# Kernel tuning notes

Measured on AMD Instinct MI355X. Metric: run time of the kernel, lower is better.

The kernel has to match this reference:

```python
import jax, jax.numpy as jnp
import numpy as np

N = 100_000      # nodes
E = 3_200_000    # edges (avg degree 32)
HID = 64         # hid_dim == in_dim
T = 4            # S2V propagation rounds


def setup_inputs() -> dict:
    key = jax.random.key(0)
    ks = jax.random.split(key, 10)
    s = lambda fan: 1.0 / np.sqrt(fan)
    return {
        "x": jax.random.normal(ks[0], (N, HID), jnp.float32),
        "x_tag": jax.random.uniform(ks[1], (N,), jnp.float32),
        "edge_attr": jax.random.uniform(ks[2], (E, 1), jnp.float32),
        "edge_index": jax.random.randint(ks[3], (2, E), 0, N, dtype=jnp.int32),
        # per-layer bias-free Linear weights (stored as [in, out])
        "W1": jax.random.normal(ks[4], (T, HID), jnp.float32),            # lin1: 1 -> hid
        "W2": jax.random.normal(ks[5], (T, HID, HID), jnp.float32) * s(HID),  # lin2: in -> hid
        "W4": jax.random.normal(ks[6], (T, HID), jnp.float32),            # lin4: 1 -> hid
        "W5": jax.random.normal(ks[7], (2 * HID, 1), jnp.float32) * s(2 * HID),  # lin5
        "W6": jax.random.normal(ks[8], (HID, HID), jnp.float32) * s(HID),  # lin6
        "W7": jax.random.normal(ks[9], (HID, HID), jnp.float32) * s(HID),  # lin7
    }


def reference(x, x_tag, edge_attr, edge_index, W1, W2, W4, W5, W6, W7):
    src = edge_index[0]  # j (message source / p3 scatter target)
    dst = edge_index[1]  # i (aggregation target)
    for l in range(T):  # fixed small layer count
        p1 = x_tag[:, None] * W1[l][None, :]                        # lin1(x_tag)  [N,HID]
        e = jax.nn.relu(edge_attr * W4[l][None, :])                  # relu(lin4(edge_attr)) [E,HID]
        aggr = jax.ops.segment_sum(x[src], dst, num_segments=N)     # add-aggregate x_j at i
        p2 = aggr @ W2[l]                                            # lin2(aggr_out)
        p3 = jax.ops.segment_sum(e, src, num_segments=N)             # scatter_add at edge_index[0]
        x = jax.nn.relu(p1 + p2 + p3)
    graph_pool = jnp.sum(x, axis=0, keepdims=True) @ W6              # [1,HID]
    nodes_vec = x @ W7                                               # [N,HID]
    cat = jnp.concatenate(
        [jnp.broadcast_to(graph_pool, (x.shape[0], graph_pool.shape[1])), nodes_vec], axis=1
    )
    Q = jax.nn.relu(cat) @ W5                                        # [N,1]
    return Q
```

## Files before the change

### kernel.cpp

```cpp
#include <hip/hip_runtime.h>

constexpr int NN  = 100000;
constexpr int NE  = 3200000;
constexpr int HID = 64;
constexpr int TL  = 4;

constexpr int BIN_SHIFT = 9;
constexpr int BIN_NODES = 1 << BIN_SHIFT;
constexpr int NBINS     = (NN + BIN_NODES - 1) / BIN_NODES;
constexpr int BINCAP    = 18944;
constexpr int TILE_E    = 2048;
constexpr int PAD       = 48;
constexpr int LROW      = 72;

typedef unsigned short ushort_t;
typedef unsigned int uint_t;
typedef __attribute__((ext_vector_type(8))) short bf16x8;
typedef __attribute__((ext_vector_type(4))) float f32x4;

__device__ __forceinline__ ushort_t f2b(float f) {
  uint_t u = __float_as_uint(f);
  u += 0x7fff + ((u >> 16) & 1);
  return (ushort_t)(u >> 16);
}
__device__ __forceinline__ float b2f(ushort_t h) {
  return __uint_as_float(((uint_t)h) << 16);
}

__global__ __launch_bounds__(256) void escatter_kernel(
    const int* __restrict__ ei, const float* __restrict__ ea,
    int* __restrict__ bincursor, uint_t* __restrict__ gbin,
    int* __restrict__ bincursor2, uint_t* __restrict__ gbin2) {
  __shared__ int hist1[256], hist2[256];
  __shared__ int base1[NBINS], base2[NBINS];
  __shared__ int offs1[NBINS], offs2[NBINS];
  __shared__ int wt1[4], wt2[4];
  __shared__ uint_t srec[TILE_E];
  __shared__ int    sdst[TILE_E];
  int tid = threadIdx.x;
  int tb = blockIdx.x * TILE_E;
  hist1[tid] = 0; hist2[tid] = 0;
  __syncthreads();
  uint_t rec1[8], rec2[8]; int bn1[8], bn2[8], rk1[8], rk2[8];
  #pragma unroll
  for (int j = 0; j < 8; ++j) {
    int e = tb + tid + j * 256;
    bn1[j] = -1; bn2[j] = -1;
    rk1[j] = 0; rk2[j] = 0; rec1[j] = 0; rec2[j] = 0;
    if (e < NE) {
      int s = ei[e];
      int d = ei[NE + e];
      uint_t q = (uint_t)(int)(ea[e] * 8388608.0f);
      bn1[j] = d >> BIN_SHIFT;
      rec1[j] = ((uint_t)s << BIN_SHIFT) | (uint_t)(d & (BIN_NODES - 1));
      rk1[j] = atomicAdd(&hist1[bn1[j]], 1);
      bn2[j] = s >> BIN_SHIFT;
      rec2[j] = (q << BIN_SHIFT) | (uint_t)(s & (BIN_NODES - 1));
      rk2[j] = atomicAdd(&hist2[bn2[j]], 1);
    }
  }
  __syncthreads();
  int c1 = hist1[tid], c2 = hist2[tid];
  int lane = tid & 63;
  int wvx = tid >> 6;
  int v1 = c1, v2 = c2;
  #pragma unroll
  for (int o = 1; o < 64; o <<= 1) {
    int t1 = __shfl_up(v1, o);
    int t2 = __shfl_up(v2, o);
    if (lane >= o) { v1 += t1; v2 += t2; }
  }
  if (lane == 63) { wt1[wvx] = v1; wt2[wvx] = v2; }
  __syncthreads();
  for (int k = 0; k < wvx; ++k) { v1 += wt1[k]; v2 += wt2[k]; }
  hist1[tid] = v1; hist2[tid] = v2;
  __syncthreads();
  if (tid < NBINS) {
    offs1[tid] = hist1[tid] - c1;
    offs2[tid] = hist2[tid] - c2;
    base1[tid] = c1 ? atomicAdd(&bincursor[tid], c1) : 0;
    base2[tid] = c2 ? atomicAdd(&bincursor2[tid], c2) : 0;
  }
  __syncthreads();
  int total1 = hist1[NBINS - 1];
  int total2 = hist2[NBINS - 1];
  #pragma unroll
  for (int j = 0; j < 8; ++j) {
    if (bn1[j] >= 0) {
      int p = offs1[bn1[j]] + rk1[j];
      int gp = base1[bn1[j]] + rk1[j];
      srec[p] = rec1[j];
      sdst[p] = (gp < BINCAP) ? (bn1[j] * BINCAP + gp) : -1;
    }
  }
  __syncthreads();
  for (int t = tid; t < total1; t += 256) {
    int g = sdst[t];
    if (g >= 0) gbin[g] = srec[t];
  }
  __syncthreads();
  #pragma unroll
  for (int j = 0; j < 8; ++j) {
    if (bn2[j] >= 0) {
      int p = offs2[bn2[j]] + rk2[j];
      int gp = base2[bn2[j]] + rk2[j];
      srec[p] = rec2[j];
      sdst[p] = (gp < BINCAP) ? (bn2[j] * BINCAP + gp) : -1;
    }
  }
  __syncthreads();
  for (int t = tid; t < total2; t += 256) {
    int g = sdst[t];
    if (g >= 0) gbin2[g] = srec[t];
  }
}

__global__ __launch_bounds__(256) void bucket_kernel(
    const uint_t* __restrict__ gbin, const int* __restrict__ bincursor,
    int* __restrict__ colidx, int* __restrict__ cnt, int cap) {
  __shared__ int cur[BIN_NODES];
  int b = blockIdx.x;
  int tid = threadIdx.x;
  for (int i = tid; i < BIN_NODES; i += 256) cur[i] = 0;
  __syncthreads();
  int cb = min(bincursor[b], BINCAP);
  const uint_t* g = gbin + (size_t)b * BINCAP;
  for (int i = tid; i < cb; i += 256) {
    uint_t r = g[i];
    int dl = (int)(r & (BIN_NODES - 1));
    int src = (int)(r >> BIN_SHIFT);
    int pos = atomicAdd(&cur[dl], 1);
    int n = (b << BIN_SHIFT) + dl;
    if (pos < cap) colidx[(size_t)n * cap + pos] = src;
  }
  __syncthreads();
  for (int i = tid; i < BIN_NODES; i += 256) {
    int n = (b << BIN_SHIFT) + i;
    if (n < NN) cnt[n] = min(cur[i], cap);
  }
  for (int gsl = tid; gsl < BIN_NODES * 64; gsl += 256) {
    int i = gsl >> 6;
    int s = gsl & 63;
    int n = (b << BIN_SHIFT) + i;
    if (n < NN && s < PAD && s >= cur[i]) colidx[(size_t)n * cap + s] = NN;
  }
}

__global__ __launch_bounds__(256) void s3bucket_kernel(
    const uint_t* __restrict__ gbin, const int* __restrict__ bincursor2,
    int* __restrict__ s3i) {
  __shared__ int acc[BIN_NODES];
  int b = blockIdx.x;
  int tid = threadIdx.x;
  for (int i = tid; i < BIN_NODES; i += 256) acc[i] = 0;
  __syncthreads();
  int cb = min(bincursor2[b], BINCAP);
  const uint_t* g = gbin + (size_t)b * BINCAP;
  for (int i = tid; i < cb; i += 256) {
    uint_t r = g[i];
    atomicAdd(&acc[r & (BIN_NODES - 1)], (int)(r >> BIN_SHIFT));
  }
  __syncthreads();
  for (int i = tid; i < BIN_NODES; i += 256) {
    int n = (b << BIN_SHIFT) + i;
    if (n < NN) s3i[n] = acc[i];
  }
}

__global__ void conv_kernel(const float* __restrict__ x, ushort_t* __restrict__ xb) {
  int i = blockIdx.x * blockDim.x + threadIdx.x;
  if (i * 4 >= NN * HID) return;
  const float4 v = *reinterpret_cast<const float4*>(&x[i * 4]);
  ushort4 o;
  o.x = f2b(v.x); o.y = f2b(v.y); o.z = f2b(v.z); o.w = f2b(v.w);
  *reinterpret_cast<ushort4*>(&xb[i * 4]) = o;
}

__global__ void wconv_kernel(const float* __restrict__ W2,
                             const float* __restrict__ W7,
                             ushort_t* __restrict__ w2t,
                             ushort_t* __restrict__ w7t) {
  int i = blockIdx.x * blockDim.x + threadIdx.x;
  int tot2 = TL * HID * HID;
  if (i < tot2) {
    int l = i >> 12, r = i & 4095, h = r >> 6, k = r & 63;
    w2t[i] = f2b(W2[(size_t)l * 4096 + k * 64 + h]);
  } else if (i < tot2 + HID * HID) {
    int j = i - tot2, h = j >> 6, k = j & 63;
    w7t[j] = f2b(W7[k * 64 + h]);
  }
}

__global__ __launch_bounds__(256) void dense_kernel(
    const ushort_t* __restrict__ xin, const ushort_t* __restrict__ wt,
    ushort_t* __restrict__ yout) {
  int lane = threadIdx.x & 63;
  int wv = (blockIdx.x * blockDim.x + threadIdx.x) >> 6;
  int n0 = wv * 32;
  if (n0 >= NN) return;
  int row = lane & 15;
  int ks = (lane >> 4) * 8;
  bf16x8 a0 = *(const bf16x8*)&xin[(size_t)(n0 + row) * HID + ks];
  bf16x8 a1 = *(const bf16x8*)&xin[(size_t)(n0 + row) * HID + 32 + ks];
  bf16x8 a2 = *(const bf16x8*)&xin[(size_t)(n0 + 16 + row) * HID + ks];
  bf16x8 a3 = *(const bf16x8*)&xin[(size_t)(n0 + 16 + row) * HID + 32 + ks];
  #pragma unroll
  for (int ct = 0; ct < 4; ++ct) {
    bf16x8 b0 = *(const bf16x8*)&wt[(ct * 16 + row) * HID + ks];
    bf16x8 b1 = *(const bf16x8*)&wt[(ct * 16 + row) * HID + 32 + ks];
    f32x4 acc0 = {0.f, 0.f, 0.f, 0.f};
    f32x4 acc1 = {0.f, 0.f, 0.f, 0.f};
    acc0 = __builtin_amdgcn_mfma_f32_16x16x32_bf16(a0, b0, acc0, 0, 0, 0);
    acc0 = __builtin_amdgcn_mfma_f32_16x16x32_bf16(a1, b1, acc0, 0, 0, 0);
    acc1 = __builtin_amdgcn_mfma_f32_16x16x32_bf16(a2, b0, acc1, 0, 0, 0);
    acc1 = __builtin_amdgcn_mfma_f32_16x16x32_bf16(a3, b1, acc1, 0, 0, 0);
    int rr = (lane >> 4) * 4;
    #pragma unroll
    for (int r = 0; r < 4; ++r) {
      yout[(size_t)(n0 + rr + r) * HID + ct * 16 + row] = f2b(acc0[r]);
      yout[(size_t)(n0 + 16 + rr + r) * HID + ct * 16 + row] = f2b(acc1[r]);
    }
  }
}

__global__ __launch_bounds__(512) void aggrf_kernel(
    const ushort_t* __restrict__ yin, ushort_t* __restrict__ out,
    const ushort_t* __restrict__ w2tn,
    const int* __restrict__ cnt, const int* __restrict__ colidx, int cap,
    const float* __restrict__ x_tag, const int* __restrict__ s3i,
    const float* __restrict__ W1l, const float* __restrict__ W4l) {
  __shared__ ushort_t sx[16 * LROW];
  int tid = threadIdx.x;
  int lane = tid & 63;
  int wv = tid >> 6;
  int n0b = blockIdx.x * 16;
  int half = lane >> 5;
  int nloc = wv * 2 + half;
  int n = n0b + nloc;
  int grp = (lane >> 3) & 3;
  int sub = lane & 7;
  const int* cl = colidx + (size_t)n * cap + grp;
  float f0 = 0.f, f1 = 0.f, f2 = 0.f, f3 = 0.f;
  float f4 = 0.f, f5 = 0.f, f6 = 0.f, f7 = 0.f;
  uint4 w[12];
  #pragma unroll
  for (int j = 0; j < 12; ++j) {
    int c = cl[j * 4];
    w[j] = *reinterpret_cast<const uint4*>(&yin[(size_t)c * HID + sub * 8]);
  }
  #pragma unroll
  for (int j = 0; j < 12; ++j) {
    f0 += __uint_as_float(w[j].x << 16);
    f1 += __uint_as_float(w[j].x & 0xffff0000u);
    f2 += __uint_as_float(w[j].y << 16);
    f3 += __uint_as_float(w[j].y & 0xffff0000u);
    f4 += __uint_as_float(w[j].z << 16);
    f5 += __uint_as_float(w[j].z & 0xffff0000u);
    f6 += __uint_as_float(w[j].w << 16);
    f7 += __uint_as_float(w[j].w & 0xffff0000u);
  }
  int deg = cnt[n];
  if (__any(deg > PAD)) {
    int t2 = deg - PAD;
    const int* ct2 = colidx + (size_t)n * cap + PAD;
    for (int jt = 0; jt < 12; ++jt) {
      int idx = jt * 4 + grp;
      if (idx < t2) {
        int c = ct2[idx];
        uint4 ww = *reinterpret_cast<const uint4*>(&yin[(size_t)c * HID + sub * 8]);
        f0 += __uint_as_float(ww.x << 16);
        f1 += __uint_as_float(ww.x & 0xffff0000u);
        f2 += __uint_as_float(ww.y << 16);
        f3 += __uint_as_float(ww.y & 0xffff0000u);
        f4 += __uint_as_float(ww.z << 16);
        f5 += __uint_as_float(ww.z & 0xffff0000u);
        f6 += __uint_as_float(ww.w << 16);
        f7 += __uint_as_float(ww.w & 0xffff0000u);
      }
    }
  }
  #pragma unroll
  for (int m = 8; m <= 16; m <<= 1) {
    f0 += __shfl_xor(f0, m); f1 += __shfl_xor(f1, m);
    f2 += __shfl_xor(f2, m); f3 += __shfl_xor(f3, m);
    f4 += __shfl_xor(f4, m); f5 += __shfl_xor(f5, m);
    f6 += __shfl_xor(f6, m); f7 += __shfl_xor(f7, m);
  }
  float xt = x_tag[n];
  float s3f = (float)s3i[n] * 0x1p-23f;
  float4 w1a = *reinterpret_cast<const float4*>(&W1l[sub * 8]);
  float4 w1b = *reinterpret_cast<const float4*>(&W1l[sub * 8 + 4]);
  float4 w4a = *reinterpret_cast<const float4*>(&W4l[sub * 8]);
  float4 w4b = *reinterpret_cast<const float4*>(&W4l[sub * 8 + 4]);
  float o0 = fmaxf(fmaf(xt, w1a.x, fmaf(s3f, fmaxf(w4a.x, 0.f), f0)), 0.f);
  float o1 = fmaxf(fmaf(xt, w1a.y, fmaf(s3f, fmaxf(w4a.y, 0.f), f1)), 0.f);
  float o2 = fmaxf(fmaf(xt, w1a.z, fmaf(s3f, fmaxf(w4a.z, 0.f), f2)), 0.f);
  float o3 = fmaxf(fmaf(xt, w1a.w, fmaf(s3f, fmaxf(w4a.w, 0.f), f3)), 0.f);
  float o4 = fmaxf(fmaf(xt, w1b.x, fmaf(s3f, fmaxf(w4b.x, 0.f), f4)), 0.f);
  float o5 = fmaxf(fmaf(xt, w1b.y, fmaf(s3f, fmaxf(w4b.y, 0.f), f5)), 0.f);
  float o6 = fmaxf(fmaf(xt, w1b.z, fmaf(s3f, fmaxf(w4b.z, 0.f), f6)), 0.f);
  float o7 = fmaxf(fmaf(xt, w1b.w, fmaf(s3f, fmaxf(w4b.w, 0.f), f7)), 0.f);
  uint4 o;
  o.x = (uint_t)f2b(o0) | ((uint_t)f2b(o1) << 16);
  o.y = (uint_t)f2b(o2) | ((uint_t)f2b(o3) << 16);
  o.z = (uint_t)f2b(o4) | ((uint_t)f2b(o5) << 16);
  o.w = (uint_t)f2b(o6) | ((uint_t)f2b(o7) << 16);
  if (w2tn) {
    if (grp == 0)
      *reinterpret_cast<uint4*>(&sx[nloc * LROW + sub * 8]) = o;
    __syncthreads();
    if (wv < 4) {
      int row = lane & 15;
      int ks = (lane >> 4) * 8;
      bf16x8 a0 = *(const bf16x8*)&sx[row * LROW + ks];
      bf16x8 a1 = *(const bf16x8*)&sx[row * LROW + 32 + ks];
      int ct = wv;
      bf16x8 b0 = *(const bf16x8*)&w2tn[(ct * 16 + row) * HID + ks];
      bf16x8 b1 = *(const bf16x8*)&w2tn[(ct * 16 + row) * HID + 32 + ks];
      f32x4 acc = {0.f, 0.f, 0.f, 0.f};
      acc = __builtin_amdgcn_mfma_f32_16x16x32_bf16(a0, b0, acc, 0, 0, 0);
      acc = __builtin_amdgcn_mfma_f32_16x16x32_bf16(a1, b1, acc, 0, 0, 0);
      int rr = (lane >> 4) * 4;
      #pragma unroll
      for (int r = 0; r < 4; ++r)
        out[(size_t)(n0b + rr + r) * HID + ct * 16 + row] = f2b(acc[r]);
    }
  } else {
    if (grp == 0)
      *reinterpret_cast<uint4*>(&out[(size_t)n * HID + sub * 8]) = o;
  }
}

__global__ __launch_bounds__(256) void qdense_kernel(
    const ushort_t* __restrict__ xin, const ushort_t* __restrict__ w7t,
    const float* __restrict__ w5hi, float* __restrict__ Qr,
    float* __restrict__ sumx) {
  __shared__ float ssum[4][HID];
  int tid = threadIdx.x;
  int lane = tid & 63;
  int wloc = tid >> 6;
  int wv = (blockIdx.x * blockDim.x + tid) >> 6;
  int n0 = wv * 16;
  bool valid = n0 < NN;
  int n0c = valid ? n0 : 0;
  int row = lane & 15;
  int g = lane >> 4;
  int ks = g * 8;
  bf16x8 a0 = *(const bf16x8*)&xin[(size_t)(n0c + row) * HID + ks];
  bf16x8 a1 = *(const bf16x8*)&xin[(size_t)(n0c + row) * HID + 32 + ks];
  float r0 = 0.f, r1 = 0.f, r2 = 0.f, r3 = 0.f;
  #pragma unroll
  for (int ct = 0; ct < 4; ++ct) {
    bf16x8 b0 = *(const bf16x8*)&w7t[(ct * 16 + row) * HID + ks];
    bf16x8 b1 = *(const bf16x8*)&w7t[(ct * 16 + row) * HID + 32 + ks];
    f32x4 acc = {0.f, 0.f, 0.f, 0.f};
    acc = __builtin_amdgcn_mfma_f32_16x16x32_bf16(a0, b0, acc, 0, 0, 0);
    acc = __builtin_amdgcn_mfma_f32_16x16x32_bf16(a1, b1, acc, 0, 0, 0);
    float w5 = w5hi[ct * 16 + row];
    r0 += fmaxf(acc[0], 0.f) * w5;
    r1 += fmaxf(acc[1], 0.f) * w5;
    r2 += fmaxf(acc[2], 0.f) * w5;
    r3 += fmaxf(acc[3], 0.f) * w5;
  }
  #pragma unroll
  for (int m = 1; m <= 8; m <<= 1) {
    r0 += __shfl_xor(r0, m); r1 += __shfl_xor(r1, m);
    r2 += __shfl_xor(r2, m); r3 += __shfl_xor(r3, m);
  }
  if (valid && row == 0) {
    int rb = n0 + g * 4;
    Qr[rb + 0] = r0; Qr[rb + 1] = r1; Qr[rb + 2] = r2; Qr[rb + 3] = r3;
  }
  float c[16];
  #pragma unroll
  for (int e = 0; e < 8; ++e) {
    c[e]     = valid ? b2f((ushort_t)a0[e]) : 0.f;
    c[8 + e] = valid ? b2f((ushort_t)a1[e]) : 0.f;
  }
  #pragma unroll
  for (int m = 1; m <= 8; m <<= 1) {
    #pragma unroll
    for (int e = 0; e < 16; ++e) c[e] += __shfl_xor(c[e], m);
  }
  if (row == 0) {
    #pragma unroll
    for (int e = 0; e < 8; ++e) {
      ssum[wloc][ks + e] = c[e];
      ssum[wloc][32 + ks + e] = c[8 + e];
    }
  }
  __syncthreads();
  if (tid < HID) {
    float s = ssum[0][tid] + ssum[1][tid] + ssum[2][tid] + ssum[3][tid];
    atomicAdd(&sumx[tid], s);
  }
}

__global__ void pool_kernel(const float* __restrict__ sumx, const float* __restrict__ W6,
                            const float* __restrict__ W5, float* __restrict__ c0) {
  int lane = threadIdx.x & 63;
  float sv = sumx[lane];
  float gp = 0.f;
  #pragma unroll
  for (int k = 0; k < HID; ++k) {
    float a = __int_as_float(__builtin_amdgcn_readlane(__float_as_int(sv), k));
    gp = fmaf(a, W6[k * HID + lane], gp);
  }
  float r = fmaxf(gp, 0.f) * W5[lane];
  #pragma unroll
  for (int m = 32; m >= 1; m >>= 1) r += __shfl_xor(r, m);
  if (lane == 0) *c0 = r;
}

__global__ void qfix_kernel(float* __restrict__ Q, const float* __restrict__ c0) {
  int i = blockIdx.x * blockDim.x + threadIdx.x;
  if (i < NN) Q[i] += *c0;
}

extern "C" void kernel_launch(void* const* d_in, const int* in_sizes, int n_in,
                              void* d_out, int out_size, void* d_ws, size_t ws_size,
                              hipStream_t stream) {
  const float* x         = (const float*)d_in[0];
  const float* x_tag     = (const float*)d_in[1];
  const float* edge_attr = (const float*)d_in[2];
  const int*   edge_index= (const int*)d_in[3];
  const float* W1        = (const float*)d_in[4];
  const float* W2        = (const float*)d_in[5];
  const float* W4        = (const float*)d_in[6];
  const float* W5        = (const float*)d_in[7];
  const float* W6        = (const float*)d_in[8];
  const float* W7        = (const float*)d_in[9];
  float* Q = (float*)d_out;

  const int QBLOCKS = ((NN / 16) * 64 + 255) / 256;
  const int NTILES  = (NE + TILE_E - 1) / TILE_E;

  char* ws = (char*)d_ws;
  size_t off = 0;
  auto alloc = [&](size_t bytes) -> void* {
    void* p = ws + off;
    off = (off + bytes + 255) & ~(size_t)255;
    return p;
  };
  int*      bincursor  = (int*)alloc(NBINS * 4);
  int*      bincursor2 = (int*)alloc(NBINS * 4);
  float*    sumx       = (float*)alloc(HID * 4);
  size_t zero_bytes = off;
  int*      s3i    = (int*)alloc(NN * 4);
  int*      cnt    = (int*)alloc(NN * 4);
  float*    c0     = (float*)alloc(4);
  ushort_t* xf     = (ushort_t*)alloc((size_t)NN * HID * 2);
  ushort_t* yb0    = (ushort_t*)alloc((size_t)(NN + 1) * HID * 2);
  ushort_t* yb1    = (ushort_t*)alloc((size_t)(NN + 1) * HID * 2);
  ushort_t* w2t    = (ushort_t*)alloc((size_t)TL * HID * HID * 2);
  ushort_t* w7t    = (ushort_t*)alloc((size_t)HID * HID * 2);
  uint_t*   gbin   = (uint_t*)alloc((size_t)NBINS * BINCAP * 4);
  uint_t*   gbin2  = (uint_t*)alloc((size_t)NBINS * BINCAP * 4);

  size_t rem = (ws_size > off) ? (ws_size - off) : 0;
  int cap = (int)(rem / ((size_t)NN * 4));
  if (cap > 96) cap = 96;
  if (cap < 64) cap = 64;
  int* colidx = (int*)alloc((size_t)NN * cap * 4);

  hipMemsetAsync(d_ws, 0, zero_bytes, stream);
  hipMemsetAsync(yb0 + (size_t)NN * HID, 0, HID * 2, stream);
  hipMemsetAsync(yb1 + (size_t)NN * HID, 0, HID * 2, stream);

  escatter_kernel<<<NTILES, 256, 0, stream>>>(edge_index, edge_attr,
                                              bincursor, gbin, bincursor2, gbin2);
  bucket_kernel<<<NBINS, 256, 0, stream>>>(gbin, bincursor, colidx, cnt, cap);
  s3bucket_kernel<<<NBINS, 256, 0, stream>>>(gbin2, bincursor2, s3i);
  conv_kernel<<<(NN * HID / 4 + 255) / 256, 256, 0, stream>>>(x, xf);
  wconv_kernel<<<((TL + 1) * HID * HID + 255) / 256, 256, 0, stream>>>(W2, W7, w2t, w7t);

  int dblocks = ((NN / 32) * 64 + 255) / 256;
  dense_kernel<<<dblocks, 256, 0, stream>>>(xf, w2t, yb0);

  int fblocks = NN / 16;
  ushort_t* ycur = yb0;
  ushort_t* ynext = yb1;
  for (int l = 0; l < TL; ++l) {
    bool last = (l == TL - 1);
    aggrf_kernel<<<fblocks, 512, 0, stream>>>(
        ycur, last ? xf : ynext,
        last ? nullptr : (w2t + (size_t)(l + 1) * HID * HID),
        cnt, colidx, cap, x_tag, s3i, W1 + l * HID, W4 + l * HID);
    ushort_t* t = ycur; ycur = ynext; ynext = t;
  }

  qdense_kernel<<<QBLOCKS, 256, 0, stream>>>(xf, w7t, W5 + HID, Q, sumx);
  pool_kernel<<<1, 64, 0, stream>>>(sumx, W6, W5, c0);
  qfix_kernel<<<(NN + 255) / 256, 256, 0, stream>>>(Q, c0);
}
```

Measured before the change: 410.7 us.

## Fuse x bf16 conversion into dense kernel; restructure edge scatter into two passes

The standalone fp32-to-bf16 conversion kernel for x is removed, and dense_kernel now loads fp32 x directly and converts it in registers. That saves one launch plus a bf16 write and read of x. The edge binning kernel now handles both bin streams one after the other, reusing one histogram and shared buffer, and its tile doubles to 4096 edges. The destination address is rebuilt from a byte-sized bin id, replacing the stored int, which cuts shared memory use. The cost is higher register pressure from 16 records per thread, and edge_index src is read twice.

```diff
diff --git a/kernel.cpp b/kernel.cpp
--- a/kernel.cpp
+++ b/kernel.cpp
@@ -9,12 +9,13 @@
 constexpr int BIN_NODES = 1 << BIN_SHIFT;
 constexpr int NBINS     = (NN + BIN_NODES - 1) / BIN_NODES;
 constexpr int BINCAP    = 18944;
-constexpr int TILE_E    = 2048;
+constexpr int TILE_E    = 4096;
 constexpr int PAD       = 48;
 constexpr int LROW      = 72;
 
 typedef unsigned short ushort_t;
 typedef unsigned int uint_t;
+typedef unsigned char uchar_t;
 typedef __attribute__((ext_vector_type(8))) short bf16x8;
 typedef __attribute__((ext_vector_type(4))) float f32x4;
 
@@ -31,87 +32,76 @@
     const int* __restrict__ ei, const float* __restrict__ ea,
     int* __restrict__ bincursor, uint_t* __restrict__ gbin,
     int* __restrict__ bincursor2, uint_t* __restrict__ gbin2) {
-  __shared__ int hist1[256], hist2[256];
-  __shared__ int base1[NBINS], base2[NBINS];
-  __shared__ int offs1[NBINS], offs2[NBINS];
-  __shared__ int wt1[4], wt2[4];
-  __shared__ uint_t srec[TILE_E];
-  __shared__ int    sdst[TILE_E];
+  __shared__ int hist[256];
+  __shared__ int base[NBINS], offs[NBINS];
+  __shared__ int wt[4];
+  __shared__ uint_t  srec[TILE_E];
+  __shared__ uchar_t sbin[TILE_E];
   int tid = threadIdx.x;
   int tb = blockIdx.x * TILE_E;
-  hist1[tid] = 0; hist2[tid] = 0;
-  __syncthreads();
-  uint_t rec1[8], rec2[8]; int bn1[8], bn2[8], rk1[8], rk2[8];
-  #pragma unroll
-  for (int j = 0; j < 8; ++j) {
-    int e = tb + tid + j * 256;
-    bn1[j] = -1; bn2[j] = -1;
-    rk1[j] = 0; rk2[j] = 0; rec1[j] = 0; rec2[j] = 0;
-    if (e < NE) {
-      int s = ei[e];
-      int d = ei[NE + e];
-      uint_t q = (uint_t)(int)(ea[e] * 8388608.0f);
-      bn1[j] = d >> BIN_SHIFT;
-      rec1[j] = ((uint_t)s << BIN_SHIFT) | (uint_t)(d & (BIN_NODES - 1));
-      rk1[j] = atomicAdd(&hist1[bn1[j]], 1);
-      bn2[j] = s >> BIN_SHIFT;
-      rec2[j] = (q << BIN_SHIFT) | (uint_t)(s & (BIN_NODES - 1));
-      rk2[j] = atomicAdd(&hist2[bn2[j]], 1);
-    }
-  }
-  __syncthreads();
-  int c1 = hist1[tid], c2 = hist2[tid];
   int lane = tid & 63;
   int wvx = tid >> 6;
-  int v1 = c1, v2 = c2;
-  #pragma unroll
-  for (int o = 1; o < 64; o <<= 1) {
-    int t1 = __shfl_up(v1, o);
-    int t2 = __shfl_up(v2, o);
-    if (lane >= o) { v1 += t1; v2 += t2; }
-  }
-  if (lane == 63) { wt1[wvx] = v1; wt2[wvx] = v2; }
-  __syncthreads();
-  for (int k = 0; k < wvx; ++k) { v1 += wt1[k]; v2 += wt2[k]; }
-  hist1[tid] = v1; hist2[tid] = v2;
-  __syncthreads();
-  if (tid < NBINS) {
-    offs1[tid] = hist1[tid] - c1;
-    offs2[tid] = hist2[tid] - c2;
-    base1[tid] = c1 ? atomicAdd(&bincursor[tid], c1) : 0;
-    base2[tid] = c2 ? atomicAdd(&bincursor2[tid], c2) : 0;
-  }
-  __syncthreads();
-  int total1 = hist1[NBINS - 1];
-  int total2 = hist2[NBINS - 1];
-  #pragma unroll
-  for (int j = 0; j < 8; ++j) {
-    if (bn1[j] >= 0) {
-      int p = offs1[bn1[j]] + rk1[j];
-      int gp = base1[bn1[j]] + rk1[j];
-      srec[p] = rec1[j];
-      sdst[p] = (gp < BINCAP) ? (bn1[j] * BINCAP + gp) : -1;
-    }
-  }
-  __syncthreads();
-  for (int t = tid; t < total1; t += 256) {
-    int g = sdst[t];
-    if (g >= 0) gbin[g] = srec[t];
-  }
-  __syncthreads();
-  #pragma unroll
-  for (int j = 0; j < 8; ++j) {
-    if (bn2[j] >= 0) {
-      int p = offs2[bn2[j]] + rk2[j];
-      int gp = base2[bn2[j]] + rk2[j];
-      srec[p] = rec2[j];
-      sdst[p] = (gp < BINCAP) ? (bn2[j] * BINCAP + gp) : -1;
-    }
-  }
-  __syncthreads();
-  for (int t = tid; t < total2; t += 256) {
-    int g = sdst[t];
-    if (g >= 0) gbin2[g] = srec[t];
+
+  for (int stream = 0; stream < 2; ++stream) {
+    hist[tid] = 0;
+    __syncthreads();
+    uint_t rec[16]; int meta[16];
+    #pragma unroll
+    for (int j = 0; j < 16; ++j) {
+      int e = tb + tid + j * 256;
+      meta[j] = -1; rec[j] = 0;
+      if (e < NE) {
+        int s = ei[e];
+        int bn, lo; uint_t hi;
+        if (stream == 0) {
+          int d = ei[NE + e];
+          bn = d >> BIN_SHIFT; lo = d & (BIN_NODES - 1);
+          hi = (uint_t)s;
+        } else {
+          bn = s >> BIN_SHIFT; lo = s & (BIN_NODES - 1);
+          hi = (uint_t)(int)(ea[e] * 8388608.0f);
+        }
+        rec[j] = (hi << BIN_SHIFT) | (uint_t)lo;
+        int rk = atomicAdd(&hist[bn], 1);
+        meta[j] = (bn << 12) | rk;
+      }
+    }
+    __syncthreads();
+    int c = hist[tid];
+    int v = c;
+    #pragma unroll
+    for (int o = 1; o < 64; o <<= 1) {
+      int t = __shfl_up(v, o);
+      if (lane >= o) v += t;
+    }
+    if (lane == 63) wt[wvx] = v;
+    __syncthreads();
+    for (int k = 0; k < wvx; ++k) v += wt[k];
+    hist[tid] = v;
+    if (tid < NBINS) {
+      offs[tid] = v - c;
+      int* cur = stream ? bincursor2 : bincursor;
+      base[tid] = c ? atomicAdd(&cur[tid], c) : 0;
+    }
+    __syncthreads();
+    int total = hist[NBINS - 1];
+    #pragma unroll
+    for (int j = 0; j < 16; ++j) {
+      if (meta[j] >= 0) {
+        int bn = meta[j] >> 12, rk = meta[j] & 4095;
+        int p = offs[bn] + rk;
+        srec[p] = rec[j];
+        sbin[p] = (uchar_t)bn;
+      }
+    }
+    __syncthreads();
+    uint_t* g = stream ? gbin2 : gbin;
+    for (int t = tid; t < total; t += 256) {
+      int b = sbin[t];
+      int gp = base[b] + (t - offs[b]);
+      if (gp < BINCAP) g[(size_t)b * BINCAP + gp] = srec[t];
+    }
+    __syncthreads();
   }
 }
 
@@ -167,15 +157,6 @@
   }
 }
 
-__global__ void conv_kernel(const float* __restrict__ x, ushort_t* __restrict__ xb) {
-  int i = blockIdx.x * blockDim.x + threadIdx.x;
-  if (i * 4 >= NN * HID) return;
-  const float4 v = *reinterpret_cast<const float4*>(&x[i * 4]);
-  ushort4 o;
-  o.x = f2b(v.x); o.y = f2b(v.y); o.z = f2b(v.z); o.w = f2b(v.w);
-  *reinterpret_cast<ushort4*>(&xb[i * 4]) = o;
-}
-
 __global__ void wconv_kernel(const float* __restrict__ W2,
                              const float* __restrict__ W7,
                              ushort_t* __restrict__ w2t,
@@ -191,8 +172,19 @@
   }
 }
 
+__device__ __forceinline__ bf16x8 ld8f(const float* p) {
+  float4 u = *reinterpret_cast<const float4*>(p);
+  float4 v = *reinterpret_cast<const float4*>(p + 4);
+  bf16x8 r;
+  r[0] = (short)f2b(u.x); r[1] = (short)f2b(u.y);
+  r[2] = (short)f2b(u.z); r[3] = (short)f2b(u.w);
+  r[4] = (short)f2b(v.x); r[5] = (short)f2b(v.y);
+  r[6] = (short)f2b(v.z); r[7] = (short)f2b(v.w);
+  return r;
+}
+
 __global__ __launch_bounds__(256) void dense_kernel(
-    const ushort_t* __restrict__ xin, const ushort_t* __restrict__ wt,
+    const float* __restrict__ xin, const ushort_t* __restrict__ wt,
     ushort_t* __restrict__ yout) {
   int lane = threadIdx.x & 63;
   int wv = (blockIdx.x * blockDim.x + threadIdx.x) >> 6;
@@ -200,10 +192,10 @@
   if (n0 >= NN) return;
   int row = lane & 15;
   int ks = (lane >> 4) * 8;
-  bf16x8 a0 = *(const bf16x8*)&xin[(size_t)(n0 + row) * HID + ks];
-  bf16x8 a1 = *(const bf16x8*)&xin[(size_t)(n0 + row) * HID + 32 + ks];
-  bf16x8 a2 = *(const bf16x8*)&xin[(size_t)(n0 + 16 + row) * HID + ks];
-  bf16x8 a3 = *(const bf16x8*)&xin[(size_t)(n0 + 16 + row) * HID + 32 + ks];
+  bf16x8 a0 = ld8f(&xin[(size_t)(n0 + row) * HID + ks]);
+  bf16x8 a1 = ld8f(&xin[(size_t)(n0 + row) * HID + 32 + ks]);
+  bf16x8 a2 = ld8f(&xin[(size_t)(n0 + 16 + row) * HID + ks]);
+  bf16x8 a3 = ld8f(&xin[(size_t)(n0 + 16 + row) * HID + 32 + ks]);
   #pragma unroll
   for (int ct = 0; ct < 4; ++ct) {
     bf16x8 b0 = *(const bf16x8*)&wt[(ct * 16 + row) * HID + ks];
@@ -471,11 +463,10 @@
                                               bincursor, gbin, bincursor2, gbin2);
   bucket_kernel<<<NBINS, 256, 0, stream>>>(gbin, bincursor, colidx, cnt, cap);
   s3bucket_kernel<<<NBINS, 256, 0, stream>>>(gbin2, bincursor2, s3i);
-  conv_kernel<<<(NN * HID / 4 + 255) / 256, 256, 0, stream>>>(x, xf);
   wconv_kernel<<<((TL + 1) * HID * HID + 255) / 256, 256, 0, stream>>>(W2, W7, w2t, w7t);
 
   int dblocks = ((NN / 32) * 64 + 255) / 256;
-  dense_kernel<<<dblocks, 256, 0, stream>>>(xf, w2t, yb0);
+  dense_kernel<<<dblocks, 256, 0, stream>>>(x, w2t, yb0);
 
   int fblocks = NN / 16;
   ushort_t* ycur = yb0;
```

New measurement: 395.0 us. 3.8% less time.
